# Kernel tuning notes

Measured on AMD Instinct MI355X. Metric: run time of the kernel, lower is better.

## Reference

```python
import jax, jax.numpy as jnp
import numpy as np
import math

L_DEG, N_PTS, T_ER, P_RAD, C_IN, C_OUT = 4, 8192, 15, 5, 16, 16


def _cg(j1, m1, j2, m2, j3, m3):
    # Clebsch-Gordan coefficient <j1 m1 j2 m2 | j3 m3> (Racah formula),
    # replacing sympy's CG(...).doit() used by the original module.
    if m1 + m2 != m3:
        return 0.0
    if j3 < abs(j1 - j2) or j3 > j1 + j2:
        return 0.0
    f = math.factorial
    pre = math.sqrt((2 * j3 + 1) * f(j3 + j1 - j2) * f(j3 - j1 + j2) * f(j1 + j2 - j3) / f(j1 + j2 + j3 + 1))
    pre *= math.sqrt(f(j3 + m3) * f(j3 - m3) * f(j1 - m1) * f(j1 + m1) * f(j2 - m2) * f(j2 + m2))
    s = 0.0
    for k in range(max(0, j2 - j3 - m1, j1 - j3 + m2), min(j1 + j2 - j3, j1 - m1, j2 + m2) + 1):
        s += (-1.0) ** k / (f(k) * f(j1 + j2 - j3 - k) * f(j1 - m1 - k) * f(j2 + m2 - k) * f(j3 - j2 + m1 + k) * f(j3 - j1 - m2 + k))
    return pre * s


def _precompute(L):
    # Mirrors PrecomputingTensorsForConv6D.
    tens, coefs = [], []
    for l in range(L):
        for l1 in range(L):
            for l2 in range(abs(l - l1), min(L, l + l1 + 1)):
                coefs.append(8.0 * np.pi ** 2 / (2 * l1 + 1)
                             * np.sqrt((2 * l + 1) * (2 * l1 + 1) / (4.0 * np.pi * (2 * l2 + 1)))
                             * _cg(l, 0, l1, 0, l2, 0))
                T1 = np.zeros((l + 1, l1 + 1, l2 + 1), np.float32)
                T2 = np.zeros_like(T1)
                T3 = np.zeros_like(T1)
                for k in range(l + 1):
                    for k1 in range(l1 + 1):
                        if k + k1 < l2 + 1:
                            T1[k, k1, k + k1] = _cg(l, k, l1, k1, l2, k + k1) * (-1) ** k1
                        if k1 > 0 and abs(k - k1) < l2 + 1:
                            if k - k1 >= 0:
                                T2[k, k1, k - k1] = _cg(l, k, l1, -k1, l2, k - k1) * (-1) ** l1
                            else:
                                T3[k, k1, k1 - k] = (-1) ** (k1 - k) * (-1) ** (l1 + l2) * _cg(l, k, l1, -k1, l2, k - k1)
                tens += [T1, T2, T3]
    return tens, [float(c) for c in coefs]


_TENS_NP, _COEFS = _precompute(L_DEG)
_TENS = [jnp.asarray(t, jnp.float32) for t in _TENS_NP]


def _forward(xs, ws, bs):
    L = L_DEG
    # zero the imaginary k=0 rows, as done via temp_term in build()
    ws_m = list(ws)
    bs_m = list(bs)
    for l in range(L):
        mk = (jnp.arange(l + 1) > 0).astype(jnp.float32)
        ws_m[2 * l + 1] = ws[2 * l + 1] * mk[:, None, None, None, None]
        bs_m[2 * l + 1] = bs[2 * l + 1] * mk[None, :, None, None]
    out = []
    itr = 0
    for l in range(L):
        o_r = 0.0
        o_i = 0.0
        for l1 in range(L):
            wr, wi = ws_m[2 * l1], ws_m[2 * l1 + 1]
            for l2 in range(abs(l - l1), min(L, l + l1 + 1)):
                c = _COEFS[itr]
                T1, T2, T3 = _TENS[3 * itr], _TENS[3 * itr + 1], _TENS[3 * itr + 2]
                xr, xi = xs[2 * l2], xs[2 * l2 + 1]
                # x: [n, t, k(l2+1), p, i]; w: [m(l1+1), t, p, i, j]; T: [l(l+1), m, k]
                o_r = o_r + c * jnp.einsum('lmk,ntkpi,mtpij->nlpj', T1 + T2 + T3, xr, wr) \
                          - c * jnp.einsum('lmk,ntkpi,mtpij->nlpj', T1 - T2 + T3, xi, wi)
                o_i = o_i + c * jnp.einsum('lmk,ntkpi,mtpij->nlpj', T1 - T2 - T3, xr, wi) \
                          + c * jnp.einsum('lmk,ntkpi,mtpij->nlpj', T1 + T2 - T3, xi, wr)
                itr += 1
        out.append(o_r + bs_m[2 * l])
        out.append(o_i + bs_m[2 * l + 1])
    return tuple(out)


def setup_inputs() -> dict:
    key = jax.random.key(0)
    ks = jax.random.split(key, 24)
    inp = {}
    i = 0
    for l in range(L_DEG):
        for part in ('r', 'i'):
            inp['x%d%s' % (l, part)] = jax.random.normal(ks[i], (N_PTS, T_ER, l + 1, P_RAD, C_IN), jnp.float32)
            i += 1
    for l in range(L_DEG):
        for part in ('r', 'i'):
            inp['w%d%s' % (l, part)] = jax.random.normal(ks[i], (l + 1, T_ER, P_RAD, C_IN, C_OUT), jnp.float32) * 0.05
            i += 1
    for l in range(L_DEG):
        for part in ('r', 'i'):
            inp['b%d%s' % (l, part)] = jax.random.normal(ks[i], (1, l + 1, P_RAD, C_OUT), jnp.float32) * 0.05
            i += 1
    return inp


def reference(x0r, x0i, x1r, x1i, x2r, x2i, x3r, x3i,
              w0r, w0i, w1r, w1i, w2r, w2i, w3r, w3i,
              b0r, b0i, b1r, b1i, b2r, b2i, b3r, b3i):
    xs = [x0r, x0i, x1r, x1i, x2r, x2i, x3r, x3i]
    ws = [w0r, w0i, w1r, w1i, w2r, w2i, w3r, w3i]
    bs = [b0r, b0i, b1r, b1i, b2r, b2i, b3r, b3i]
    return _forward(xs, ws, bs)
```

## Files before the change

### kernel.cpp

```cpp
#include <hip/hip_runtime.h>

#define PI_D 3.14159265358979323846


typedef __attribute__((ext_vector_type(8))) short short8;
typedef __attribute__((ext_vector_type(4))) float f32x4;

struct Ptrs8 { const float* p[8]; };

__device__ __forceinline__ ushort f2bf(float x){
  uint u = __float_as_uint(x);
  return (ushort)((u + 0x7fffu + ((u>>16)&1u)) >> 16);
}

__device__ __forceinline__ double dfact(int n){ double r=1.0; for(int i=2;i<=n;++i) r*=(double)i; return r; }

__device__ double cg_coef(int j1,int m1,int j2,int m2,int j3,int m3){
  if(m1+m2!=m3) return 0.0;
  if(j3<abs(j1-j2)||j3>j1+j2) return 0.0;
  if(abs(m1)>j1||abs(m2)>j2||abs(m3)>j3) return 0.0;
  double pre = sqrt((2.0*j3+1.0)*dfact(j3+j1-j2)*dfact(j3-j1+j2)*dfact(j1+j2-j3)/dfact(j1+j2+j3+1));
  pre *= sqrt(dfact(j3+m3)*dfact(j3-m3)*dfact(j1-m1)*dfact(j1+m1)*dfact(j2-m2)*dfact(j2+m2));
  int kmin = max(0,max(j2-j3-m1,j1-j3+m2));
  int kmax = min(j1+j2-j3,min(j1-m1,j2+m2));
  double s=0.0;
  for(int k=kmin;k<=kmax;++k){
    double d = dfact(k)*dfact(j1+j2-j3-k)*dfact(j1-m1-k)*dfact(j2+m2-k)*dfact(j3-j2+m1+k)*dfact(j3-j1-m2+k);
    s += ((k&1)?-1.0:1.0)/d;
  }
  return pre*s;
}

__device__ __forceinline__ int gidx(int l,int l2,int combo,int lr,int kx,int l1,int m){
  return ((((((l*4+l2)*4+combo)*4+lr)*4+kx)*4+l1)*4+m);
}

__global__ void g_kernel(float* __restrict__ G){
  int tid = threadIdx.x;
  for(int e=tid;e<16384;e+=blockDim.x) G[e]=0.0f;
  __syncthreads();
  int trip = tid >> 4;
  int sub  = tid & 15;
  int lr = sub >> 2, m = sub & 3;
  int idx=0;
  for(int l=0;l<4;l++)for(int l1=0;l1<4;l1++){
    int lo=abs(l-l1), hi=min(3,l+l1);
    for(int l2=lo;l2<=hi;l2++){
      if(idx==trip && lr<=l && m<=l1){
        double c = 8.0*PI_D*PI_D/(2.0*l1+1.0)
                 * sqrt((2.0*l+1.0)*(2.0*l1+1.0)/(4.0*PI_D*(2.0*l2+1.0)))
                 * cg_coef(l,0,l1,0,l2,0);
        if(lr+m<=l2){
          float f = (float)(c * cg_coef(l,lr,l1,m,l2,lr+m) * ((m&1)?-1.0:1.0));
          G[gidx(l,l2,0,lr,lr+m,l1,m)] += f;
          G[gidx(l,l2,1,lr,lr+m,l1,m)] -= f;
          G[gidx(l,l2,2,lr,lr+m,l1,m)] += f;
          G[gidx(l,l2,3,lr,lr+m,l1,m)] += f;
        }
        if(m>0 && abs(lr-m)<=l2){
          if(lr-m>=0){
            float f = (float)(c * cg_coef(l,lr,l1,-m,l2,lr-m) * ((l1&1)?-1.0:1.0));
            G[gidx(l,l2,0,lr,lr-m,l1,m)] += f;
            G[gidx(l,l2,1,lr,lr-m,l1,m)] += f;
            G[gidx(l,l2,2,lr,lr-m,l1,m)] -= f;
            G[gidx(l,l2,3,lr,lr-m,l1,m)] += f;
          } else {
            float f = (float)(c * (((m-lr)&1)?-1.0:1.0) * (((l1+l2)&1)?-1.0:1.0)
                              * cg_coef(l,lr,l1,-m,l2,lr-m));
            G[gidx(l,l2,0,lr,m-lr,l1,m)] += f;
            G[gidx(l,l2,1,lr,m-lr,l1,m)] -= f;
            G[gidx(l,l2,2,lr,m-lr,l1,m)] -= f;
            G[gidx(l,l2,3,lr,m-lr,l1,m)] -= f;
          }
        }
      }
      idx++;
    }
  }
}

__device__ __forceinline__ void decode_kb(int kb,int& l2,int& partp,int& kx,int& t){
  int kbo;
  if(kb<30){l2=0;kbo=0;} else if(kb<90){l2=1;kbo=30;} else if(kb<180){l2=2;kbo=90;} else {l2=3;kbo=180;}
  int rem = kb-kbo;
  int per = (l2+1)*15;
  partp = rem/per;
  int q = rem%per;
  kx = q/15; t = q%15;
}

__device__ __forceinline__ void decode_col(int col,int& l,int& part,int& lr,int& j){
  int co;
  if(col<32){l=0;co=0;} else if(col<96){l=1;co=32;} else if(col<192){l=2;co=96;} else {l=3;co=192;}
  int cr = col-co; int per=(l+1)*16;
  part = cr/per; int q = cr%per; lr = q>>4; j = q&15;
}

__global__ void w_kernel(const float* __restrict__ G, Ptrs8 wp, ushort* __restrict__ W){
  long e = (long)blockIdx.x*256 + threadIdx.x;
  if(e >= 5L*320*4800) return;
  int K = (int)(e%4800); long r = e/4800; int col = (int)(r%320); int p = (int)(r/320);
  int i = K & 15; int kb = K >> 4;
  int l2,partp,kx,t; decode_kb(kb,l2,partp,kx,t);
  int l,part,lr,j; decode_col(col,l,part,lr,j);
  int combo = (part==0) ? (partp==0?0:1) : (partp==0?2:3);
  int wpart = (combo==0||combo==3)?0:1;
  int mstart = wpart?1:0;
  int woff = t*1280 + p*256 + i*16 + j;
  float acc=0.f;
  for(int l1=0;l1<4;l1++){
    const float* wptr = wp.p[l1*2+wpart];
    int gb = ((((l*4+l2)*4+combo)*4+lr)*4+kx)*16 + l1*4;
    for(int m=mstart;m<=l1;m++){
      float g = G[gb+m];
      if(g!=0.f) acc += g * wptr[m*19200 + woff];
    }
  }
  W[e] = f2bf(acc);
}


__device__ __forceinline__ void a_load(const Ptrs8& xp, int p, int n0, int kt, int w, int lane, float4* v){
  int kb = kt*4 + w;
  int l2,partp,kx,t; decode_kb(kb,l2,partp,kx,t);
  const float* xb = xp.p[l2*2+partp];
  int nstr = 1200*(l2+1);
  const float* base = xb + (long)(n0 + (lane>>2))*nstr + (t*(l2+1)+kx)*80 + p*16 + (lane&3)*4;
  long step = (long)16*nstr;
  #pragma unroll
  for(int s=0;s<4;++s) v[s] = *(const float4*)(base + s*step);
}

__device__ __forceinline__ void a_store(ushort* As, int w, int lane, const float4* v){
  int rsub = lane>>2, c4 = (lane&3)*4;
  #pragma unroll
  for(int s=0;s<4;++s){
    int row = s*16 + rsub;
    int e = row*64 + ((w*16 + c4) ^ ((row&7)<<3));
    uint2 d;
    d.x = (uint)f2bf(v[s].x) | ((uint)f2bf(v[s].y)<<16);
    d.y = (uint)f2bf(v[s].z) | ((uint)f2bf(v[s].w)<<16);
    *(uint2*)(As + e) = d;
  }
}

__device__ __forceinline__ void b_load(const ushort* Wp, int w, int lane, int kt, short8* b){
  const ushort* q = Wp + (long)(w*80 + (lane&15))*4800 + kt*64 + ((lane>>4)*8);
  #pragma unroll
  for(int ks=0;ks<2;++ks)
    #pragma unroll
    for(int ni=0;ni<5;++ni)
      b[ks*5+ni] = *(const short8*)(q + (long)ni*16*4800 + ks*32);
}

__device__ __forceinline__ void do_mfma(const ushort* As, int lane, const short8* b, f32x4 acc[4][5]){
  #pragma unroll
  for(int ks=0;ks<2;++ks){
    short8 af[4];
    #pragma unroll
    for(int mi=0;mi<4;++mi){
      int row = mi*16 + (lane&15);
      int e = row*64 + (((ks*32) + (lane>>4)*8) ^ ((row&7)<<3));
      af[mi] = *(const short8*)(As + e);
    }
    #pragma unroll
    for(int mi=0;mi<4;++mi)
      #pragma unroll
      for(int ni=0;ni<5;++ni)
        acc[mi][ni] = __builtin_amdgcn_mfma_f32_16x16x32_bf16(af[mi], b[ks*5+ni], acc[mi][ni], 0,0,0);
  }
}

__global__ __launch_bounds__(256,2) void gemm_kernel(Ptrs8 xp, const ushort* __restrict__ Wb,
                                                     Ptrs8 bp, float* __restrict__ out){
  __shared__ ushort As[2][4096];
  const int tid = threadIdx.x;
  const int lane = tid & 63;
  const int w = tid >> 6;
  const int nb = blockIdx.x, p = blockIdx.y;
  const int n0 = nb*64;
  const ushort* Wp = Wb + (long)p*320*4800;

  f32x4 acc[4][5] = {};
  float4 av[4];
  short8 bfr[10];

  a_load(xp, p, n0, 0, w, lane, av);
  a_store(&As[0][0], w, lane, av);
  b_load(Wp, w, lane, 0, bfr);
  __syncthreads();

  int buf = 0;
  #pragma unroll 1
  for(int kt=0;kt<74;++kt){
    a_load(xp, p, n0, kt+1, w, lane, av);
    do_mfma(&As[buf][0], lane, bfr, acc);
    b_load(Wp, w, lane, kt+1, bfr);
    a_store(&As[buf^1][0], w, lane, av);
    __syncthreads();
    buf ^= 1;
  }
  do_mfma(&As[buf][0], lane, bfr, acc);

  int j = lane & 15, rg = (lane>>4)*4;
  #pragma unroll
  for(int ni=0;ni<5;++ni){
    int col16 = w*5 + ni;
    int l, part, lr;
    if(col16<2){l=0;part=col16;lr=0;}
    else if(col16<6){int c=col16-2;l=1;part=c>>1;lr=c&1;}
    else if(col16<12){int c=col16-6;l=2;part=(c>=3);lr=part?(c-3):c;}
    else {int c=col16-12;l=3;part=c>>2;lr=c&3;}
    float bv = 0.f;
    if(!(part==1 && lr==0)) bv = bp.p[l*2+part][lr*80 + p*16 + j];
    long base = 655360L*(l+1)*(l+part);
    int nst = (l+1)*80;
    long ioff = base + lr*80 + p*16 + j;
    #pragma unroll
    for(int mi=0;mi<4;++mi){
      int n = n0 + mi*16 + rg;
      #pragma unroll
      for(int r=0;r<4;++r)
        out[ioff + (long)(n+r)*nst] = acc[mi][ni][r] + bv;
    }
  }
}

extern "C" void kernel_launch(void* const* d_in, const int* in_sizes, int n_in,
                              void* d_out, int out_size, void* d_ws, size_t ws_size,
                              hipStream_t stream){
  Ptrs8 xp, wp, bp;
  for(int i=0;i<8;i++){
    xp.p[i] = (const float*)d_in[i];
    wp.p[i] = (const float*)d_in[8+i];
    bp.p[i] = (const float*)d_in[16+i];
  }
  float* G = (float*)d_ws;
  ushort* W = (ushort*)((char*)d_ws + 16384*4);
  g_kernel<<<dim3(1), dim3(576), 0, stream>>>(G);
  w_kernel<<<dim3(30000), dim3(256), 0, stream>>>(G, wp, W);
  gemm_kernel<<<dim3(128,5), dim3(256), 0, stream>>>(xp, W, bp, (float*)d_out);
}
```

Baseline: 495.1 us.

## Deepen GEMM software pipeline with register double-buffering and XCD-aware block remap

The GEMM main loop now prefetches A tiles two k-steps ahead and B fragments one step ahead, using ping-pong register sets and a manually unrolled pair of steps. The goal is to hide global-load latency behind the MFMA work. The __syncthreads is replaced by a raw barrier that waits only on LDS traffic, and s_setprio raises wave priority around the MFMA section. The 2D grid becomes a 1D grid with a remap that spreads consecutive blocks across the 8 XCDs, so blocks sharing a p slice share L2. In exchange, register pressure rises from the doubled buffers, which could spill or lower occupancy under launch_bounds(256,2).

```diff
diff --git a/kernel.cpp b/kernel.cpp
--- a/kernel.cpp
+++ b/kernel.cpp
@@ -8,9 +8,9 @@
 
 struct Ptrs8 { const float* p[8]; };
 
-__device__ __forceinline__ ushort f2bf(float x){
+__device__ __forceinline__ uint f2bf(float x){
   uint u = __float_as_uint(x);
-  return (ushort)((u + 0x7fffu + ((u>>16)&1u)) >> 16);
+  return ((u + 0x7fffu + ((u>>16)&1u)) >> 16);
 }
 
 __device__ __forceinline__ double dfact(int n){ double r=1.0; for(int i=2;i<=n;++i) r*=(double)i; return r; }
@@ -116,11 +116,11 @@
       if(g!=0.f) acc += g * wptr[m*19200 + woff];
     }
   }
-  W[e] = f2bf(acc);
-}
-
-
-__device__ __forceinline__ void a_load(const Ptrs8& xp, int p, int n0, int kt, int w, int lane, float4* v){
+  W[e] = (ushort)f2bf(acc);
+}
+
+
+__device__ __forceinline__ void a_issue(const Ptrs8& xp,int p,int n0,int kt,int w,int lane,float4* v){
   int kb = kt*4 + w;
   int l2,partp,kx,t; decode_kb(kb,l2,partp,kx,t);
   const float* xb = xp.p[l2*2+partp];
@@ -131,20 +131,20 @@
   for(int s=0;s<4;++s) v[s] = *(const float4*)(base + s*step);
 }
 
-__device__ __forceinline__ void a_store(ushort* As, int w, int lane, const float4* v){
+__device__ __forceinline__ void a_store(ushort* As,int w,int lane,const float4* v){
   int rsub = lane>>2, c4 = (lane&3)*4;
   #pragma unroll
   for(int s=0;s<4;++s){
     int row = s*16 + rsub;
     int e = row*64 + ((w*16 + c4) ^ ((row&7)<<3));
     uint2 d;
-    d.x = (uint)f2bf(v[s].x) | ((uint)f2bf(v[s].y)<<16);
-    d.y = (uint)f2bf(v[s].z) | ((uint)f2bf(v[s].w)<<16);
+    d.x = f2bf(v[s].x) | (f2bf(v[s].y)<<16);
+    d.y = f2bf(v[s].z) | (f2bf(v[s].w)<<16);
     *(uint2*)(As + e) = d;
   }
 }
 
-__device__ __forceinline__ void b_load(const ushort* Wp, int w, int lane, int kt, short8* b){
+__device__ __forceinline__ void b_load(const ushort* Wp,int w,int lane,int kt,short8* b){
   const ushort* q = Wp + (long)(w*80 + (lane&15))*4800 + kt*64 + ((lane>>4)*8);
   #pragma unroll
   for(int ks=0;ks<2;++ks)
@@ -153,7 +153,7 @@
       b[ks*5+ni] = *(const short8*)(q + (long)ni*16*4800 + ks*32);
 }
 
-__device__ __forceinline__ void do_mfma(const ushort* As, int lane, const short8* b, f32x4 acc[4][5]){
+__device__ __forceinline__ void do_mfma(const ushort* As,int lane,const short8* b,f32x4 acc[4][5]){
   #pragma unroll
   for(int ks=0;ks<2;++ks){
     short8 af[4];
@@ -170,6 +170,12 @@
         acc[mi][ni] = __builtin_amdgcn_mfma_f32_16x16x32_bf16(af[mi], b[ks*5+ni], acc[mi][ni], 0,0,0);
   }
 }
+
+#define RAW_BAR() do { \
+  asm volatile("s_waitcnt lgkmcnt(0)" ::: "memory"); \
+  __builtin_amdgcn_s_barrier(); \
+  __builtin_amdgcn_sched_barrier(0); \
+} while(0)
 
 __global__ __launch_bounds__(256,2) void gemm_kernel(Ptrs8 xp, const ushort* __restrict__ Wb,
                                                      Ptrs8 bp, float* __restrict__ out){
@@ -177,30 +183,42 @@
   const int tid = threadIdx.x;
   const int lane = tid & 63;
   const int w = tid >> 6;
-  const int nb = blockIdx.x, p = blockIdx.y;
+  int orig = blockIdx.x;
+  int wg = (orig & 7)*80 + (orig >> 3);
+  const int p = wg / 128;
+  const int nb = wg % 128;
   const int n0 = nb*64;
   const ushort* Wp = Wb + (long)p*320*4800;
 
   f32x4 acc[4][5] = {};
-  float4 av[4];
-  short8 bfr[10];
-
-  a_load(xp, p, n0, 0, w, lane, av);
-  a_store(&As[0][0], w, lane, av);
-  b_load(Wp, w, lane, 0, bfr);
-  __syncthreads();
-
-  int buf = 0;
+  float4 avA[4], avB[4];
+  short8 bfA[10], bfB[10];
+
+  a_issue(xp, p, n0, 0, w, lane, avB);
+  a_store(&As[0][0], w, lane, avB);
+  a_issue(xp, p, n0, 1, w, lane, avA);
+  b_load(Wp, w, lane, 0, bfA);
+  RAW_BAR();
+
+#define STEP(kt, avIn, avOut, bIn, bOut) do { \
+    if((kt) < 73) a_issue(xp, p, n0, (kt)+2, w, lane, avOut); \
+    b_load(Wp, w, lane, (kt)+1, bOut); \
+    __builtin_amdgcn_s_setprio(1); \
+    do_mfma(&As[(kt)&1][0], lane, bIn, acc); \
+    __builtin_amdgcn_s_setprio(0); \
+    a_store(&As[((kt)+1)&1][0], w, lane, avIn); \
+    RAW_BAR(); \
+  } while(0)
+
   #pragma unroll 1
-  for(int kt=0;kt<74;++kt){
-    a_load(xp, p, n0, kt+1, w, lane, av);
-    do_mfma(&As[buf][0], lane, bfr, acc);
-    b_load(Wp, w, lane, kt+1, bfr);
-    a_store(&As[buf^1][0], w, lane, av);
-    __syncthreads();
-    buf ^= 1;
-  }
-  do_mfma(&As[buf][0], lane, bfr, acc);
+  for(int kt=0; kt<74; kt+=2){
+    STEP(kt,   avA, avB, bfA, bfB);
+    STEP(kt+1, avB, avA, bfB, bfA);
+  }
+  __builtin_amdgcn_s_setprio(1);
+  do_mfma(&As[0][0], lane, bfA, acc);
+  __builtin_amdgcn_s_setprio(0);
+#undef STEP
 
   int j = lane & 15, rg = (lane>>4)*4;
   #pragma unroll
@@ -239,5 +257,5 @@
   ushort* W = (ushort*)((char*)d_ws + 16384*4);
   g_kernel<<<dim3(1), dim3(576), 0, stream>>>(G);
   w_kernel<<<dim3(30000), dim3(256), 0, stream>>>(G, wp, W);
-  gemm_kernel<<<dim3(128,5), dim3(256), 0, stream>>>(xp, W, bp, (float*)d_out);
-}
+  gemm_kernel<<<dim3(640), dim3(256), 0, stream>>>(xp, W, bp, (float*)d_out);
+}
```

After: 537.3 us. 8.5% more time.
